# Performance work log

Hardware: AMD Instinct MI355X
Metric: run time of the kernel (lower is better)

The kernel has to match this reference:

```python
import jax, jax.numpy as jnp
import numpy as np

N, E = 50000, 800000
IN_DIM, NHID, HEADS, OUT_DIM = 256, 32, 4, 128
NEG_SLOPE = 0.2


def gat_conv(x, src, dst, W, a_src, a_dst, bias, heads, out_ch, concat):
    """PyG-style GATConv (eval mode, self-loops already included in src/dst)."""
    n = x.shape[0]
    h = (x @ W).reshape(n, heads, out_ch)                  # [N, H, C]
    alpha_s = jnp.einsum('nhc,hc->nh', h, a_src)           # [N, H]
    alpha_d = jnp.einsum('nhc,hc->nh', h, a_dst)           # [N, H]
    e = jax.nn.leaky_relu(alpha_s[src] + alpha_d[dst], NEG_SLOPE)  # [Etot, H]
    # softmax over incoming edges of each destination node
    m = jax.ops.segment_max(e, dst, num_segments=n)
    e = jnp.exp(e - m[dst])
    s = jax.ops.segment_sum(e, dst, num_segments=n)
    alpha = e / (s[dst] + 1e-16)                           # [Etot, H]
    msg = h[src] * alpha[:, :, None]                       # [Etot, H, C]
    out = jax.ops.segment_sum(msg, dst, num_segments=n)    # [N, H, C]
    out = out.reshape(n, heads * out_ch) if concat else out.mean(axis=1)
    return out + bias


def setup_inputs() -> dict:
    key = jax.random.key(0)
    ks = jax.random.split(key, 11)
    g = lambda k, shape, fan: jax.random.normal(k, shape, jnp.float32) * (1.0 / np.sqrt(fan))
    x = jax.random.normal(ks[0], (N, IN_DIM), jnp.float32)
    edge_index = jax.random.randint(ks[1], (2, E), 0, N, dtype=jnp.int32)
    return {
        'x': x,
        'edge_index': edge_index,
        'W1': g(ks[2], (IN_DIM, HEADS * NHID), IN_DIM),
        'att_src1': g(ks[3], (HEADS, NHID), NHID),
        'att_dst1': g(ks[4], (HEADS, NHID), NHID),
        'b1': jnp.zeros((HEADS * NHID,), jnp.float32),
        'W2': g(ks[5], (HEADS * NHID, OUT_DIM), HEADS * NHID),
        'att_src2': g(ks[6], (1, OUT_DIM), OUT_DIM),
        'att_dst2': g(ks[7], (1, OUT_DIM), OUT_DIM),
        'b2': jnp.zeros((OUT_DIM,), jnp.float32),
    }


def reference(x, edge_index, W1, att_src1, att_dst1, b1, W2, att_src2, att_dst2, b2):
    n = x.shape[0]
    # add self-loops (PyG GATConv default)
    loop = jnp.arange(n, dtype=edge_index.dtype)
    src = jnp.concatenate([edge_index[0], loop])
    dst = jnp.concatenate([edge_index[1], loop])
    # dropout(p=0.6) is identity at eval time
    h = gat_conv(x, src, dst, W1, att_src1, att_dst1, b1, HEADS, NHID, concat=True)
    h = jax.nn.elu(h)
    out = gat_conv(h, src, dst, W2, att_src2, att_dst2, b2, 1, OUT_DIM, concat=False)
    return out
```

## Files before the change

### kernel.cpp

```cpp
#include <hip/hip_runtime.h>
#include <hip/hip_bf16.h>
#include <type_traits>

typedef __hip_bfloat16 bf16;

#define IN_DIM 256
#define NHID 32
#define HEADS 4
#define OUT_DIM 128
#define HC 128
#define SLOT 96

typedef __attribute__((ext_vector_type(8))) __bf16 bf16x8_t;
typedef __attribute__((ext_vector_type(2))) __bf16 bf16x2_t;
typedef __attribute__((ext_vector_type(2))) _Float16 f16x2_t;
typedef __attribute__((ext_vector_type(4))) float f32x4_t;

__device__ __forceinline__ float bf2f(bf16 v) { return __bfloat162float(v); }

__global__ void k_detect(const unsigned int* __restrict__ x, int* __restrict__ flag) {
    int t = threadIdx.x;
    int cnt = 0;
    for (int i = t; i < 4096; i += 256) {
        unsigned u = x[(size_t)i * 64];
        unsigned e = (u >> 7) & 0xFF;
        cnt += (e >= 100 && e < 130) ? 1 : 0;
    }
    __shared__ int sh[256];
    sh[t] = cnt;
    __syncthreads();
    for (int off = 128; off > 0; off >>= 1) {
        if (t < off) sh[t] += sh[t + off];
        __syncthreads();
    }
    if (t == 0) *flag = (sh[0] < 2048) ? 1 : 0;
}

struct CvtSrcs { const void* p[8]; };

__global__ void k_cvt_all(CvtSrcs srcs, float* __restrict__ dst0,
                          const int* __restrict__ flag) {
    const int cum[9] = {0, 32768, 32896, 33024, 33152, 49536, 49664, 49792, 49920};
    int i = blockIdx.x * 256 + threadIdx.x;
    if (i >= 49920) return;
    int jb = 0;
#pragma unroll
    for (int k = 1; k < 8; k++) jb += (i >= cum[k]) ? 1 : 0;
    int off = i - cum[jb];
    const void* sp = srcs.p[0];
#pragma unroll
    for (int k = 1; k < 8; k++) if (jb == k) sp = srcs.p[k];
    float v;
    if (*flag) v = ((const float*)sp)[off];
    else v = bf2f(((const bf16*)sp)[off]);
    dst0[i] = v;
}

__global__ void k_prep_panel(const float* __restrict__ w, __bf16* __restrict__ bt,
                             int K, int reps_hi, int nseg) {
    int total = 128 * K * nseg;
    int i = blockIdx.x * 256 + threadIdx.x;
    if (i >= total) return;
    int c = i / (K * nseg);
    int kp = i - c * (K * nseg);
    int seg = kp / K, ksrc = kp - seg * K;
    float v = w[ksrc * 128 + c];
    __bf16 h = (__bf16)v;
    bt[i] = (seg < reps_hi) ? h : (__bf16)(v - (float)h);
}

__global__ void k_fill_slot(const int* __restrict__ src, const int* __restrict__ dst,
                            int E, int* __restrict__ deg,
                            unsigned short* __restrict__ slots) {
    int base = (blockIdx.x * blockDim.x + threadIdx.x) * 4;
    if (base + 4 <= E) {
        int4 d4 = *(const int4*)(dst + base);
        int4 s4 = *(const int4*)(src + base);
        int dd[4] = {d4.x, d4.y, d4.z, d4.w};
        int ss[4] = {s4.x, s4.y, s4.z, s4.w};
#pragma unroll
        for (int k = 0; k < 4; k++) {
            int pos = atomicAdd(&deg[dd[k]], 1);
            if (pos < SLOT) slots[(size_t)dd[k] * SLOT + pos] = (unsigned short)ss[k];
        }
    } else {
        for (int e = base; e < E; e++) {
            int d = dst[e];
            int pos = atomicAdd(&deg[d], 1);
            if (pos < SLOT) slots[(size_t)d * SLOT + pos] = (unsigned short)src[e];
        }
    }
}


template <int MODE>
__device__ __forceinline__ int a_off(int ks) {
    if constexpr (MODE == 0)
        return (ks < 8) ? ks * 64 : (ks < 16) ? 512 + (ks - 8) * 64 : (ks - 16) * 64;
    else if constexpr (MODE == 1)
        return (ks & 7) * 64;
    else
        return (ks < 4) ? ks * 64 : (ks < 8) ? 256 + (ks - 4) * 64 : (ks - 8) * 64;
}

template <int MODE>
__global__ void __launch_bounds__(256, 3)
k_gemm(const void* __restrict__ A_, const __bf16* __restrict__ B,
       _Float16* __restrict__ C, int n, const int* __restrict__ flag, int want) {
    if (want >= 0 && *flag != want) return;
    if (n <= 0) return;
    constexpr int NKS  = (MODE == 0) ? 24 : (MODE == 1) ? 16 : 12;
    constexpr int NH   = NKS / 2;
    constexpr int ROWB = (MODE == 0) ? 1024 : 512;
    constexpr int BSTR = NKS * 64;
    __shared__ __align__(16) char lds[32 * ROWB];
    const int t = threadIdx.x;
    const int row0 = blockIdx.x * 32;

    const int wave = t >> 6, lane = t & 63;
    const int l15 = lane & 15, lg = lane >> 4;
    const char* bp0 = (const char*)B + (size_t)(wave * 32 + l15) * BSTR + lg * 16;
    const char* bp1 = (const char*)B + (size_t)(wave * 32 + 16 + l15) * BSTR + lg * 16;

    if constexpr (MODE == 0) {
        const float* A = (const float*)A_;
#pragma unroll
        for (int r = 0; r < 4; r++) {
            int idx = r * 256 + t;
            int row = idx >> 5, k8 = idx & 31;
            int gr = row0 + row; if (gr > n - 1) gr = n - 1;
            const float* p = A + (size_t)gr * 256 + k8 * 8;
            float4 v0 = *(const float4*)p;
            float4 v1 = *(const float4*)(p + 4);
            float v[8] = {v0.x, v0.y, v0.z, v0.w, v1.x, v1.y, v1.z, v1.w};
            bf16x8_t hi, lo;
#pragma unroll
            for (int j = 0; j < 8; j++) {
                __bf16 h = (__bf16)v[j];
                hi[j] = h;
                lo[j] = (__bf16)(v[j] - (float)h);
            }
            int sw = (row & 7) << 4;
            *(bf16x8_t*)(lds + row * 1024 + ((k8 * 16) ^ sw)) = hi;
            *(bf16x8_t*)(lds + row * 1024 + ((512 + k8 * 16) ^ sw)) = lo;
        }
    } else {
        const __bf16* A = (const __bf16*)A_;
#pragma unroll
        for (int r = 0; r < 4; r++) {
            int idx = r * 256 + t;
            int row = idx >> 5, k8 = idx & 31;
            int gr = row0 + row; if (gr > n - 1) gr = n - 1;
            bf16x8_t v = *(const bf16x8_t*)(A + (size_t)gr * 256 + k8 * 8);
            int sw = (row & 7) << 4;
            *(bf16x8_t*)(lds + row * 512 + ((k8 * 16) ^ sw)) = v;
        }
    }

    bf16x8_t br0[NH], br1[NH];
#pragma unroll
    for (int i = 0; i < NH; i++) {
        br0[i] = *(const bf16x8_t*)(bp0 + i * 64);
        br1[i] = *(const bf16x8_t*)(bp1 + i * 64);
    }
    __builtin_amdgcn_sched_barrier(0);

    __syncthreads();

    const int sw = (l15 & 7) << 4;
    const char* ar0 = lds + l15 * ROWB;
    const char* ar1 = lds + (16 + l15) * ROWB;

    f32x4_t acc[2][2];
#pragma unroll
    for (int rt = 0; rt < 2; rt++)
#pragma unroll
        for (int ct = 0; ct < 2; ct++)
            acc[rt][ct] = (f32x4_t){0.f, 0.f, 0.f, 0.f};

#pragma unroll
    for (int i = 0; i < NH; i++) {
        int ao = a_off<MODE>(i) + lg * 16;
        bf16x8_t a0 = *(const bf16x8_t*)(ar0 + (ao ^ sw));
        bf16x8_t a1 = *(const bf16x8_t*)(ar1 + (ao ^ sw));
        acc[0][0] = __builtin_amdgcn_mfma_f32_16x16x32_bf16(a0, br0[i], acc[0][0], 0, 0, 0);
        acc[0][1] = __builtin_amdgcn_mfma_f32_16x16x32_bf16(a0, br1[i], acc[0][1], 0, 0, 0);
        acc[1][0] = __builtin_amdgcn_mfma_f32_16x16x32_bf16(a1, br0[i], acc[1][0], 0, 0, 0);
        acc[1][1] = __builtin_amdgcn_mfma_f32_16x16x32_bf16(a1, br1[i], acc[1][1], 0, 0, 0);
    }

#pragma unroll
    for (int i = 0; i < NH; i++) {
        br0[i] = *(const bf16x8_t*)(bp0 + (NH + i) * 64);
        br1[i] = *(const bf16x8_t*)(bp1 + (NH + i) * 64);
    }
    __builtin_amdgcn_sched_barrier(0);

#pragma unroll
    for (int i = 0; i < NH; i++) {
        int ao = a_off<MODE>(NH + i) + lg * 16;
        bf16x8_t a0 = *(const bf16x8_t*)(ar0 + (ao ^ sw));
        bf16x8_t a1 = *(const bf16x8_t*)(ar1 + (ao ^ sw));
        acc[0][0] = __builtin_amdgcn_mfma_f32_16x16x32_bf16(a0, br0[i], acc[0][0], 0, 0, 0);
        acc[0][1] = __builtin_amdgcn_mfma_f32_16x16x32_bf16(a0, br1[i], acc[0][1], 0, 0, 0);
        acc[1][0] = __builtin_amdgcn_mfma_f32_16x16x32_bf16(a1, br0[i], acc[1][0], 0, 0, 0);
        acc[1][1] = __builtin_amdgcn_mfma_f32_16x16x32_bf16(a1, br1[i], acc[1][1], 0, 0, 0);
    }

#pragma unroll
    for (int rt = 0; rt < 2; rt++) {
#pragma unroll
        for (int r = 0; r < 4; r++) {
            int row = row0 + rt * 16 + lg * 4 + r;
            if (row < n) {
#pragma unroll
                for (int ct = 0; ct < 2; ct++) {
                    int colx = wave * 32 + ct * 16 + l15;
                    C[(size_t)row * 128 + colx] = (_Float16)acc[rt][ct][r];
                }
            }
        }
    }
}


template <int H, int C>
__global__ void k_alpha(const _Float16* __restrict__ h, const float* __restrict__ a_src,
                        const float* __restrict__ a_dst, int n,
                        float* __restrict__ as, float* __restrict__ ad) {
    int i = blockIdx.x * blockDim.x + threadIdx.x;
    if (i >= n * H) return;
    int node = i / H, hh = i - node * H;
    const f16x2_t* hp = (const f16x2_t*)(h + (size_t)node * (H * C) + hh * C);
    float ss = 0.f, sd = 0.f;
#pragma unroll
    for (int c = 0; c < C / 2; c++) {
        f16x2_t v = hp[c];
        float f0 = (float)v[0], f1 = (float)v[1];
        ss += f0 * a_src[hh * C + 2 * c] + f1 * a_src[hh * C + 2 * c + 1];
        sd += f0 * a_dst[hh * C + 2 * c] + f1 * a_dst[hh * C + 2 * c + 1];
    }
    as[i] = ss;
    ad[i] = sd;
}


template <int H, int C, bool ELU_OUT, int OMODE>
__global__ void __launch_bounds__(256)
k_agg(const _Float16* __restrict__ feat,
      const float* __restrict__ as,
      const float* __restrict__ ad,
      const int* __restrict__ deg,
      const unsigned short* __restrict__ slots,
      const float* __restrict__ bias,
      void* __restrict__ out_, int n,
      const int* __restrict__ flag) {
    constexpr int HC_ = H * C;
    const int wid = threadIdx.x >> 6;
    const int l = threadIdx.x & 63;
    const int node = blockIdx.x * 4 + wid;
    __shared__ float p_lds[4][H * 65];
    __shared__ int s_lds[4][64];
    if (node >= n) return;
    const int fdt = (OMODE == 3) ? *flag : 0;
    const int hg = (2 * l) / C;
    const int hg65 = hg * 65;
    float ad_reg[H];
    if constexpr (H == 4) {
        float4 a4 = *(const float4*)(ad + (size_t)node * 4);
        ad_reg[0] = a4.x; ad_reg[1] = a4.y; ad_reg[2] = a4.z; ad_reg[3] = a4.w;
    } else {
        ad_reg[0] = ad[node];
    }
    const unsigned short* sl = slots + (size_t)node * SLOT;
    int dg = deg[node]; if (dg > SLOT) dg = SLOT;
    const int total = dg + 1;
    float acc0 = 0.f, acc1 = 0.f;
    float s_loc[H];
#pragma unroll
    for (int hh = 0; hh < H; hh++) s_loc[hh] = 0.f;

    for (int base = 0; base < total; base += 64) {
        const int cl = min(64, total - base);
        if (l < cl) {
            int j = base + l;
            int s = (j < total - 1) ? (int)sl[j] : node;
            s_lds[wid][l] = s;
            if constexpr (H == 4) {
                float4 a4 = *(const float4*)(as + (size_t)s * 4);
                float av[4] = {a4.x, a4.y, a4.z, a4.w};
#pragma unroll
                for (int hh = 0; hh < 4; hh++) {
                    float e = av[hh] + ad_reg[hh];
                    e = (e > 0.f) ? e : 0.2f * e;
                    float p = __expf(e);
                    p_lds[wid][hh * 65 + l] = p;
                    s_loc[hh] += p;
                }
            } else {
                float e = as[s] + ad_reg[0];
                e = (e > 0.f) ? e : 0.2f * e;
                float p = __expf(e);
                p_lds[wid][l] = p;
                s_loc[0] += p;
            }
        }
        asm volatile("s_waitcnt lgkmcnt(0)" ::: "memory");
        __builtin_amdgcn_sched_barrier(0);
        int j = 0;
        for (; j + 4 <= cl; j += 4) {
            int s0 = s_lds[wid][j], s1 = s_lds[wid][j + 1];
            int s2 = s_lds[wid][j + 2], s3 = s_lds[wid][j + 3];
            float w0 = p_lds[wid][hg65 + j],     w1 = p_lds[wid][hg65 + j + 1];
            float w2 = p_lds[wid][hg65 + j + 2], w3 = p_lds[wid][hg65 + j + 3];
            f16x2_t v0 = *(const f16x2_t*)(feat + (size_t)s0 * HC_ + 2 * l);
            f16x2_t v1 = *(const f16x2_t*)(feat + (size_t)s1 * HC_ + 2 * l);
            f16x2_t v2 = *(const f16x2_t*)(feat + (size_t)s2 * HC_ + 2 * l);
            f16x2_t v3 = *(const f16x2_t*)(feat + (size_t)s3 * HC_ + 2 * l);
            acc0 += w0 * (float)v0[0] + w1 * (float)v1[0] + w2 * (float)v2[0] + w3 * (float)v3[0];
            acc1 += w0 * (float)v0[1] + w1 * (float)v1[1] + w2 * (float)v2[1] + w3 * (float)v3[1];
        }
        for (; j < cl; j++) {
            int s = s_lds[wid][j];
            float w = p_lds[wid][hg65 + j];
            f16x2_t v = *(const f16x2_t*)(feat + (size_t)s * HC_ + 2 * l);
            acc0 += w * (float)v[0];
            acc1 += w * (float)v[1];
        }
        asm volatile("s_waitcnt lgkmcnt(0)" ::: "memory");
        __builtin_amdgcn_sched_barrier(0);
    }

    float r[H];
#pragma unroll
    for (int hh = 0; hh < H; hh++) {
        float v = s_loc[hh];
#pragma unroll
        for (int off = 32; off > 0; off >>= 1) v += __shfl_xor(v, off);
        r[hh] = v;
    }
    float den;
    if constexpr (H == 1) den = r[0];
    else den = (hg == 0) ? r[0] : (hg == 1) ? r[1] : (hg == 2) ? r[2] : r[3];
    float inv = 1.f / (den + 1e-16f);
    float2 bv = *(const float2*)(bias + 2 * l);
    float v0f = acc0 * inv + bv.x;
    float v1f = acc1 * inv + bv.y;
    if (ELU_OUT) {
        v0f = (v0f > 0.f) ? v0f : expm1f(v0f);
        v1f = (v1f > 0.f) ? v1f : expm1f(v1f);
    }
    if constexpr (OMODE == 2) {
        __bf16 h0 = (__bf16)v0f, h1 = (__bf16)v1f;
        bf16x2_t hi; hi[0] = h0; hi[1] = h1;
        bf16x2_t lo; lo[0] = (__bf16)(v0f - (float)h0); lo[1] = (__bf16)(v1f - (float)h1);
        bf16x2_t* o = (bf16x2_t*)out_;
        o[(size_t)node * 128 + l] = hi;
        o[(size_t)node * 128 + 64 + l] = lo;
    } else {
        if (fdt) {
            ((float2*)out_)[(size_t)node * 64 + l] = make_float2(v0f, v1f);
        } else {
            bf16x2_t ob; ob[0] = (__bf16)v0f; ob[1] = (__bf16)v1f;
            ((bf16x2_t*)out_)[(size_t)node * 64 + l] = ob;
        }
    }
}


extern "C" void kernel_launch(void* const* d_in, const int* in_sizes, int n_in,
                              void* d_out, int out_size, void* d_ws, size_t ws_size,
                              hipStream_t stream) {
    const void* x  = d_in[0];
    const int*  ei = (const int*)d_in[1];

    int n = in_sizes[0] / IN_DIM;
    int E = in_sizes[1] / 2;
    const int* src = ei;
    const int* dst = ei + E;

    char* w = (char*)d_ws;
    auto alloc = [&](size_t bytes) -> void* {
        void* p = (void*)w;
        w += (bytes + 255) / 256 * 256;
        return p;
    };
    int*      flag   = (int*)alloc(256);
    float*    w1f    = (float*)alloc((size_t)IN_DIM * HC * 4);
    float*    as1w   = (float*)alloc(HEADS * NHID * 4);
    float*    ad1w   = (float*)alloc(HEADS * NHID * 4);
    float*    b1f    = (float*)alloc(HC * 4);
    float*    w2f    = (float*)alloc((size_t)HC * OUT_DIM * 4);
    float*    as2w   = (float*)alloc(OUT_DIM * 4);
    float*    ad2w   = (float*)alloc(OUT_DIM * 4);
    float*    b2f    = (float*)alloc(OUT_DIM * 4);
    __bf16*   bf1    = (__bf16*)alloc((size_t)128 * 768 * 2);
    __bf16*   bb1    = (__bf16*)alloc((size_t)128 * 512 * 2);
    __bf16*   b2p    = (__bf16*)alloc((size_t)128 * 384 * 2);
    _Float16* h16    = (_Float16*)alloc((size_t)n * HC * 2);
    float*    hmid   = (float*)alloc((size_t)n * HC * 4);
    float*    as1    = (float*)alloc((size_t)n * HEADS * 4);
    float*    ad1    = (float*)alloc((size_t)n * HEADS * 4);
    float*    as2    = (float*)alloc((size_t)n * 4);
    float*    ad2    = (float*)alloc((size_t)n * 4);
    int*      deg    = (int*)alloc((size_t)n * 4);
    unsigned short* slots = (unsigned short*)alloc((size_t)n * SLOT * 2);
    __bf16*   a2 = (__bf16*)hmid;

    k_detect<<<1, 256, 0, stream>>>((const unsigned int*)x, flag);

    CvtSrcs srcs;
    srcs.p[0] = d_in[2]; srcs.p[1] = d_in[3]; srcs.p[2] = d_in[4]; srcs.p[3] = d_in[5];
    srcs.p[4] = d_in[6]; srcs.p[5] = d_in[7]; srcs.p[6] = d_in[8]; srcs.p[7] = d_in[9];
    k_cvt_all<<<(49920 + 255) / 256, 256, 0, stream>>>(srcs, w1f, flag);

    k_prep_panel<<<(128 * 768 + 255) / 256, 256, 0, stream>>>(w1f, bf1, 256, 2, 3);
    k_prep_panel<<<(128 * 512 + 255) / 256, 256, 0, stream>>>(w1f, bb1, 256, 1, 2);
    k_prep_panel<<<(128 * 384 + 255) / 256, 256, 0, stream>>>(w2f, b2p, 128, 2, 3);

    hipMemsetAsync(deg, 0, (size_t)n * 4, stream);

    int nfb = (E / 4 + 255) / 256 + 1;
    k_fill_slot<<<nfb, 256, 0, stream>>>(src, dst, E, deg, slots);

    int gg = (n + 31) / 32;
    k_gemm<1><<<gg, 256, 0, stream>>>(x, bb1, h16, n, flag, 0);
    k_gemm<0><<<gg, 256, 0, stream>>>(x, bf1, h16, n, flag, 1);
    k_alpha<HEADS, NHID><<<((size_t)n * HEADS + 255) / 256, 256, 0, stream>>>(h16, as1w, ad1w, n, as1, ad1);
    k_agg<HEADS, NHID, true, 2><<<(n + 3) / 4, 256, 0, stream>>>(
        h16, as1, ad1, deg, slots, b1f, a2, n, flag);

    k_gemm<2><<<gg, 256, 0, stream>>>(a2, b2p, h16, n, flag, -1);
    k_alpha<1, OUT_DIM><<<(n + 255) / 256, 256, 0, stream>>>(h16, as2w, ad2w, n, as2, ad2);
    k_agg<1, OUT_DIM, false, 3><<<(n + 3) / 4, 256, 0, stream>>>(
        h16, as2, ad2, deg, slots, b2f, d_out, n, flag);
}
```

Before: 327.2 us.

## Pre-swizzle weight panel into MFMA fragment order and reorder GEMM global loads

The weight panel prep kernel now writes B in a layout where each 1 KB unit holds one MFMA fragment for a wave, laid out as lane-contiguous 16-byte pieces. That lets the GEMM fetch B with fully coalesced loads instead of strided per-row reads. The GEMM also issues all A global loads into registers first, then the first half of the B loads, then does the bf16 conversion and LDS stores, so the load latencies overlap. The added registers for the staged A data could lower occupancy under the 3-blocks-per-SM launch bound.

```diff
diff --git a/kernel.cpp b/kernel.cpp
--- a/kernel.cpp
+++ b/kernel.cpp
@@ -58,11 +58,18 @@
 
 __global__ void k_prep_panel(const float* __restrict__ w, __bf16* __restrict__ bt,
                              int K, int reps_hi, int nseg) {
+    int NKS = nseg * K / 32;
     int total = 128 * K * nseg;
     int i = blockIdx.x * 256 + threadIdx.x;
     if (i >= total) return;
-    int c = i / (K * nseg);
-    int kp = i - c * (K * nseg);
+    int e = i & 7;  int r = i >> 3;
+    int lg = r & 3; r >>= 2;
+    int l15 = r & 15; r >>= 4;
+    int ct = r & 1; r >>= 1;
+    int ks = r % NKS;
+    int wc = r / NKS;
+    int c = wc * 32 + ct * 16 + l15;
+    int kp = ks * 32 + lg * 8 + e;
     int seg = kp / K, ksrc = kp - seg * K;
     float v = w[ksrc * 128 + c];
     __bf16 h = (__bf16)v;
@@ -112,16 +119,16 @@
     constexpr int NKS  = (MODE == 0) ? 24 : (MODE == 1) ? 16 : 12;
     constexpr int NH   = NKS / 2;
     constexpr int ROWB = (MODE == 0) ? 1024 : 512;
-    constexpr int BSTR = NKS * 64;
     __shared__ __align__(16) char lds[32 * ROWB];
     const int t = threadIdx.x;
     const int row0 = blockIdx.x * 32;
-
     const int wave = t >> 6, lane = t & 63;
     const int l15 = lane & 15, lg = lane >> 4;
-    const char* bp0 = (const char*)B + (size_t)(wave * 32 + l15) * BSTR + lg * 16;
-    const char* bp1 = (const char*)B + (size_t)(wave * 32 + 16 + l15) * BSTR + lg * 16;
-
+
+    const char* bunit = (const char*)B + (size_t)wave * NKS * 2 * 1024 + l15 * 64 + lg * 16;
+
+    float4 vaf[8];
+    bf16x8_t vab[4];
     if constexpr (MODE == 0) {
         const float* A = (const float*)A_;
 #pragma unroll
@@ -130,9 +137,34 @@
             int row = idx >> 5, k8 = idx & 31;
             int gr = row0 + row; if (gr > n - 1) gr = n - 1;
             const float* p = A + (size_t)gr * 256 + k8 * 8;
-            float4 v0 = *(const float4*)p;
-            float4 v1 = *(const float4*)(p + 4);
-            float v[8] = {v0.x, v0.y, v0.z, v0.w, v1.x, v1.y, v1.z, v1.w};
+            vaf[2 * r]     = *(const float4*)p;
+            vaf[2 * r + 1] = *(const float4*)(p + 4);
+        }
+    } else {
+        const __bf16* A = (const __bf16*)A_;
+#pragma unroll
+        for (int r = 0; r < 4; r++) {
+            int idx = r * 256 + t;
+            int row = idx >> 5, k8 = idx & 31;
+            int gr = row0 + row; if (gr > n - 1) gr = n - 1;
+            vab[r] = *(const bf16x8_t*)(A + (size_t)gr * 256 + k8 * 8);
+        }
+    }
+    __builtin_amdgcn_sched_barrier(0);
+
+    bf16x8_t br0[NH], br1[NH];
+#pragma unroll
+    for (int i = 0; i < NH; i++)
+        br0[i] = *(const bf16x8_t*)(bunit + (size_t)(2 * i) * 1024);
+    __builtin_amdgcn_sched_barrier(0);
+
+    if constexpr (MODE == 0) {
+#pragma unroll
+        for (int r = 0; r < 4; r++) {
+            int idx = r * 256 + t;
+            int row = idx >> 5, k8 = idx & 31;
+            float v[8] = {vaf[2 * r].x, vaf[2 * r].y, vaf[2 * r].z, vaf[2 * r].w,
+                          vaf[2 * r + 1].x, vaf[2 * r + 1].y, vaf[2 * r + 1].z, vaf[2 * r + 1].w};
             bf16x8_t hi, lo;
 #pragma unroll
             for (int j = 0; j < 8; j++) {
@@ -145,24 +177,18 @@
             *(bf16x8_t*)(lds + row * 1024 + ((512 + k8 * 16) ^ sw)) = lo;
         }
     } else {
-        const __bf16* A = (const __bf16*)A_;
 #pragma unroll
         for (int r = 0; r < 4; r++) {
             int idx = r * 256 + t;
             int row = idx >> 5, k8 = idx & 31;
-            int gr = row0 + row; if (gr > n - 1) gr = n - 1;
-            bf16x8_t v = *(const bf16x8_t*)(A + (size_t)gr * 256 + k8 * 8);
             int sw = (row & 7) << 4;
-            *(bf16x8_t*)(lds + row * 512 + ((k8 * 16) ^ sw)) = v;
-        }
-    }
-
-    bf16x8_t br0[NH], br1[NH];
-#pragma unroll
-    for (int i = 0; i < NH; i++) {
-        br0[i] = *(const bf16x8_t*)(bp0 + i * 64);
-        br1[i] = *(const bf16x8_t*)(bp1 + i * 64);
-    }
+            *(bf16x8_t*)(lds + row * 512 + ((k8 * 16) ^ sw)) = vab[r];
+        }
+    }
+
+#pragma unroll
+    for (int i = 0; i < NH; i++)
+        br1[i] = *(const bf16x8_t*)(bunit + (size_t)(2 * i + 1) * 1024);
     __builtin_amdgcn_sched_barrier(0);
 
     __syncthreads();
@@ -191,8 +217,8 @@
 
 #pragma unroll
     for (int i = 0; i < NH; i++) {
-        br0[i] = *(const bf16x8_t*)(bp0 + (NH + i) * 64);
-        br1[i] = *(const bf16x8_t*)(bp1 + (NH + i) * 64);
+        br0[i] = *(const bf16x8_t*)(bunit + (size_t)(2 * (NH + i)) * 1024);
+        br1[i] = *(const bf16x8_t*)(bunit + (size_t)(2 * (NH + i) + 1) * 1024);
     }
     __builtin_amdgcn_sched_barrier(0);
 
```

After: 299.0 us. -8.6%, faster.
